# Performance work log

Hardware: AMD Instinct MI355X
Metric: run time of the kernel (lower is better)

The kernel has to match this reference:

```python
import jax, jax.numpy as jnp
from jax import lax
import numpy as np

BINS = 25
K = 5  # entropy patch size
EPS = 1e-5


def conv2d(x, w, b, stride, pad):
    y = lax.conv_general_dilated(x, w, (stride, stride), [(pad, pad), (pad, pad)],
                                 dimension_numbers=("NCHW", "OIHW", "NCHW"))
    return y + b[None, :, None, None]


def group_norm_per_channel(x, w, b):
    # GroupNorm with num_groups == num_channels: per-channel norm over H,W (biased var)
    mu = x.mean(axis=(2, 3), keepdims=True)
    v = x.var(axis=(2, 3), keepdims=True)
    return (x - mu) / jnp.sqrt(v + EPS) * w[None, :, None, None] + b[None, :, None, None]


def channel_entropy(x):
    # x: (b,c,h,w). Unfold into 5x5 patches, per-patch histc(bins=25) over patch
    # values using that patch's min/max range (torch.histc default), then entropy.
    b, c, h, w = x.shape
    ho, wo = h - K + 1, w - K + 1
    # (b,c,K*K,L) -- fixed 25-position loop, vectorized over all data dims
    patches = jnp.stack([x[:, :, i:i + ho, j:j + wo]
                         for i in range(K) for j in range(K)], axis=2)
    patches = patches.reshape(b, c, K * K, ho * wo)
    mn = patches.min(axis=2, keepdims=True)
    mx = patches.max(axis=2, keepdims=True)
    rng = jnp.where(mx > mn, mx - mn, jnp.ones_like(mx))
    bins = jnp.clip(jnp.floor((patches - mn) / rng * BINS), 0, BINS - 1).astype(jnp.int32)
    # histogram via comparison one-hot: (b,c,L,BINS)
    counts = (bins[..., None] == jnp.arange(BINS, dtype=jnp.int32)).sum(axis=2)
    pk = counts.astype(x.dtype) / (K * K)
    ent = (-pk * jnp.log(jnp.clip(pk, 1e-5, 1.0 - 1e-5))).sum(axis=-1).mean(axis=-1)  # (b,c)
    return ent[:, :, None, None]


def instance_norm_ent(x, w, b):
    ent = channel_entropy(lax.stop_gradient(x))
    mu = x.mean(axis=(2, 3), keepdims=True)
    n = x.shape[2] * x.shape[3]
    v = x.var(axis=(2, 3), keepdims=True) * (n / (n - 1))  # unbiased var (torch default)
    return (x - mu) / jnp.sqrt(v + EPS) * w[None, :, None, None] * ent + b[None, :, None, None]


def setup_inputs() -> dict:
    key = jax.random.key(0)
    ks = jax.random.split(key, 24)
    s = 0.05
    d = {
        "x": jax.random.normal(ks[0], (64, 3, 224, 224), jnp.float32),
        "conv0_w": jax.random.normal(ks[1], (8, 3, 7, 7), jnp.float32) * s,
        "conv0_b": jax.random.normal(ks[2], (8,), jnp.float32) * s,
        "conv1_w": jax.random.normal(ks[3], (16, 8, 5, 5), jnp.float32) * s,
        "conv1_b": jax.random.normal(ks[4], (16,), jnp.float32) * s,
        "conv2_w": jax.random.normal(ks[5], (32, 16, 3, 3), jnp.float32) * s,
        "conv2_b": jax.random.normal(ks[6], (32,), jnp.float32) * s,
        "gn0_w": jnp.ones((8,), jnp.float32) + jax.random.normal(ks[7], (8,), jnp.float32) * s,
        "gn0_b": jax.random.normal(ks[8], (8,), jnp.float32) * s,
        "n1_w": jnp.ones((16,), jnp.float32) + jax.random.normal(ks[9], (16,), jnp.float32) * s,
        "n1_b": jax.random.normal(ks[10], (16,), jnp.float32) * s,
        "n2_w": jnp.ones((32,), jnp.float32) + jax.random.normal(ks[11], (32,), jnp.float32) * s,
        "n2_b": jax.random.normal(ks[12], (32,), jnp.float32) * s,
        "bn_g": jnp.ones((10368,), jnp.float32) + jax.random.normal(ks[13], (10368,), jnp.float32) * s,
        "bn_b": jax.random.normal(ks[14], (10368,), jnp.float32) * s,
        "fc1_w": jax.random.normal(ks[15], (32, 10368), jnp.float32) * 0.01,
        "fc1_b": jax.random.normal(ks[16], (32,), jnp.float32) * s,
        "shape_w": jax.random.normal(ks[17], (5, 32), jnp.float32) * s,
        "shape_b": jax.random.normal(ks[18], (5,), jnp.float32) * s,
        "vern_w": jax.random.normal(ks[19], (2, 32), jnp.float32) * s,
        "vern_b": jax.random.normal(ks[20], (2,), jnp.float32) * s,
    }
    return d


def reference(x, conv0_w, conv0_b, conv1_w, conv1_b, conv2_w, conv2_b,
              gn0_w, gn0_b, n1_w, n1_b, n2_w, n2_b,
              bn_g, bn_b, fc1_w, fc1_b, shape_w, shape_b, vern_w, vern_b):
    h = conv2d(x, conv0_w, conv0_b, 4, 2)          # (b,8,56,56)
    h = jax.nn.relu(group_norm_per_channel(h, gn0_w, gn0_b))
    h = conv2d(h, conv1_w, conv1_b, 3, 1)          # (b,16,18,18)
    h = jax.nn.relu(instance_norm_ent(h, n1_w, n1_b))
    h = conv2d(h, conv2_w, conv2_b, 1, 1)          # (b,32,18,18)
    h = jax.nn.relu(instance_norm_ent(h, n2_w, n2_b))
    h = h.reshape(h.shape[0], -1)                  # (b,10368)
    # BatchNorm1d (training mode: batch stats, biased var)
    mu = h.mean(axis=0)
    v = h.var(axis=0)
    h = (h - mu) / jnp.sqrt(v + EPS) * bn_g + bn_b
    h = jax.nn.relu(h @ fc1_w.T + fc1_b)           # (b,32)
    out_shape = jax.nn.softmax(h @ shape_w.T + shape_b, axis=-1)
    out_vern = jax.nn.softmax(h @ vern_w.T + vern_b, axis=-1)
    return (out_shape, out_vern)
```

## Files before the change

### kernel.cpp

```cpp
#include <hip/hip_runtime.h>
#include <math.h>

#define EPSD 1e-5


__device__ __forceinline__ double waveReduceSumD(double v) {
#pragma unroll
    for (int off = 32; off > 0; off >>= 1)
        v += __shfl_down(v, off, 64);
    return v;
}

template <int NW>
__device__ __forceinline__ double blockReduceSumD(double v, double* buf) {
    int lane = threadIdx.x & 63;
    int w = threadIdx.x >> 6;
    v = waveReduceSumD(v);
    __syncthreads();
    if (lane == 0) buf[w] = v;
    __syncthreads();
    double tot = 0.0;
#pragma unroll
    for (int i = 0; i < NW; i++) tot += buf[i];
    return tot;
}

__device__ __forceinline__ void build_ent_tab(float* tab) {
    int t = threadIdx.x;
    if (t < 26) {
        if (t == 0) tab[0] = 0.f;
        else {
            double pk = (double)t / 25.0;
            double cl = fmin(fmax(pk, 1e-5), 1.0 - 1e-5);
            tab[t] = (float)(-pk * log(cl));
        }
    }
}

__device__ __forceinline__ float patch_ent(const float* ch, int py, int px, const float* tab) {
    float pv[25];
#pragma unroll
    for (int i = 0; i < 5; i++)
#pragma unroll
        for (int j = 0; j < 5; j++)
            pv[i * 5 + j] = ch[(py + i) * 18 + px + j];
    float mn = pv[0], mx = pv[0];
#pragma unroll
    for (int k = 1; k < 25; k++) { mn = fminf(mn, pv[k]); mx = fmaxf(mx, pv[k]); }
    float rng = (mx > mn) ? (mx - mn) : 1.0f;
    unsigned long long a0 = 0ull, a1 = 0ull;
    int a2 = 0;
#pragma unroll
    for (int k = 0; k < 25; k++) {
        float tt = (pv[k] - mn) / rng * 25.0f;
        int bi = (int)floorf(tt);
        bi = bi < 0 ? 0 : (bi > 24 ? 24 : bi);
        unsigned sh0 = ((unsigned)(5 * bi)) & 63u;
        unsigned sh1 = ((unsigned)(5 * bi - 60)) & 63u;
        a0 += (bi < 12) ? (1ull << sh0) : 0ull;
        a1 += (bi >= 12 && bi < 24) ? (1ull << sh1) : 0ull;
        a2 += (bi == 24) ? 1 : 0;
    }
    float ent = 0.f;
#pragma unroll
    for (int k = 0; k < 12; k++) ent += tab[(a0 >> (5 * k)) & 31ull];
#pragma unroll
    for (int k = 0; k < 12; k++) ent += tab[(a1 >> (5 * k)) & 31ull];
    ent += tab[a2];
    return ent;
}

__global__ __launch_bounds__(128, 4) void k_conv0(const float* __restrict__ x,
                                                  const float* __restrict__ w,
                                                  const float* __restrict__ bias,
                                                  float* __restrict__ h0raw,
                                                  double* __restrict__ part0) {
    __shared__ __align__(16) float tile[2508];
    __shared__ double redbuf[2][16];
    int tl = blockIdx.x;
    int b = blockIdx.y;
    int t = threadIdx.x;
    for (int i = t; i < 2508; i += 128) tile[i] = 0.f;
    int y_base = tl * 8 - 2;
    const float* xb = x + (size_t)b * 150528;
    float acc[8];
#pragma unroll
    for (int c = 0; c < 8; c++) acc[c] = bias[c];
    int ry = t / 56, ox = t % 56;
    for (int ci = 0; ci < 3; ci++) {
        __syncthreads();
        for (int i = t; i < 616; i += 128) {
            int r = i / 56, f4 = i % 56;
            int yIn = y_base + r;
            if (yIn >= 0 && yIn < 224) {
                float4 v = *(const float4*)&xb[ci * 50176 + yIn * 224 + f4 * 4];
                float* tp = tile + r * 228;
                tp[114 + f4] = v.x;
                tp[171 + f4] = v.y;
                tp[f4 + 1]   = v.z;
                tp[58 + f4]  = v.w;
            }
        }
        __syncthreads();
        if (t < 112) {
            const float* wci = w + ci * 49;
#pragma unroll
            for (int ky = 0; ky < 7; ky++) {
                const float* rp = tile + (4 * ry + ky) * 228;
#pragma unroll
                for (int kx = 0; kx < 7; kx++) {
                    float v = rp[(kx & 3) * 57 + ox + (kx >> 2)];
#pragma unroll
                    for (int c = 0; c < 8; c++)
                        acc[c] += v * wci[c * 147 + ky * 7 + kx];
                }
            }
        }
    }
    if (t < 112) {
        int oy = tl * 2 + ry;
        int opix = oy * 56 + ox;
#pragma unroll
        for (int c = 0; c < 8; c++)
            h0raw[((size_t)b * 8 + c) * 3136 + opix] = acc[c];
    } else {
#pragma unroll
        for (int c = 0; c < 8; c++) acc[c] = 0.f;
    }
    int wv = t >> 6, lane = t & 63;
#pragma unroll
    for (int c = 0; c < 8; c++) {
        double rs = waveReduceSumD((double)acc[c]);
        double rq = waveReduceSumD((double)acc[c] * (double)acc[c]);
        if (lane == 0) { redbuf[wv][c * 2] = rs; redbuf[wv][c * 2 + 1] = rq; }
    }
    __syncthreads();
    if (t < 16) {
        double tot = redbuf[0][t] + redbuf[1][t];
        part0[(((size_t)b * 28 + tl) << 4) + t] = tot;
    }
}

__global__ __launch_bounds__(1024) void k_conv1_ent(const float* __restrict__ h0raw,
                                                    const double* __restrict__ part0,
                                                    const float* __restrict__ gw,
                                                    const float* __restrict__ gb,
                                                    const float* __restrict__ w,
                                                    const float* __restrict__ bias,
                                                    const float* __restrict__ nw,
                                                    const float* __restrict__ nb,
                                                    float* __restrict__ h1) {
    __shared__ __align__(16) float xin2[25088];
    __shared__ float vals[1296];
    __shared__ float tab[26];
    __shared__ float gnp[16];
    __shared__ double redbuf[16][2];
    __shared__ double entbuf[16];
    __shared__ float prm[4][3];
    int b = blockIdx.x >> 2;
    int grp = blockIdx.x & 3;
    int t = threadIdx.x;
    if (t < 8) {
        double s = 0.0, s2 = 0.0;
        const double* p = part0 + ((size_t)b * 28) * 16;
        for (int tile = 0; tile < 28; tile++) {
            s += p[tile * 16 + t * 2];
            s2 += p[tile * 16 + t * 2 + 1];
        }
        double mean = s / 3136.0;
        double var = s2 / 3136.0 - mean * mean;
        double rstd = 1.0 / sqrt(var + EPSD);
        double sc = (double)gw[t] * rstd;
        gnp[t] = (float)sc;
        gnp[8 + t] = (float)((double)gb[t] - mean * sc);
    }
    build_ent_tab(tab);
    __syncthreads();
    for (int i = t; i < 25088; i += 1024) {
        int ci = i / 3136, px = i - ci * 3136;
        float v = fmaxf(h0raw[(size_t)b * 25088 + i] * gnp[ci] + gnp[8 + ci], 0.f);
        xin2[(ci >> 1) * 6272 + px * 2 + (ci & 1)] = v;
    }
    __syncthreads();

    int wv = t >> 6, lane = t & 63;
    int c = wv >> 2;
    int q = wv & 3;
    int j_u = __builtin_amdgcn_readfirstlane(grp * 4 + c);
    const float* wg = w + (size_t)j_u * 200;
    float* vch = vals + c * 324;
    float bv = bias[j_u];
    double s = 0.0, s2 = 0.0;
    for (int p = q * 81 + lane; p < q * 81 + 81; p += 64) {
        int oy = p / 18, ox = p - oy * 18;
        int y0 = oy * 3 - 1, x0 = ox * 3 - 1;
        float acc = bv;
        if (oy >= 1 && ox >= 1) {
#pragma unroll
            for (int c2 = 0; c2 < 4; c2++) {
                const float* xp = xin2 + c2 * 6272 + (y0 * 56 + x0) * 2;
                const float* wp0 = wg + (2 * c2) * 25;
#pragma unroll
                for (int ky = 0; ky < 5; ky++)
#pragma unroll
                    for (int kx = 0; kx < 5; kx++) {
                        float2 v = *(const float2*)&xp[(ky * 56 + kx) * 2];
                        acc += v.x * wp0[ky * 5 + kx];
                        acc += v.y * wp0[25 + ky * 5 + kx];
                    }
            }
        } else {
            int ky0 = y0 < 0 ? 1 : 0;
            int kx0 = x0 < 0 ? 1 : 0;
            for (int c2 = 0; c2 < 4; c2++) {
                const float* xp = xin2 + c2 * 6272;
                const float* wp0 = wg + (2 * c2) * 25;
                for (int ky = ky0; ky < 5; ky++) {
                    for (int kx = kx0; kx < 5; kx++) {
                        float2 v = *(const float2*)&xp[((y0 + ky) * 56 + x0 + kx) * 2];
                        acc += v.x * wp0[ky * 5 + kx];
                        acc += v.y * wp0[25 + ky * 5 + kx];
                    }
                }
            }
        }
        vch[p] = acc;
        s += (double)acc; s2 += (double)acc * (double)acc;
    }
    s = waveReduceSumD(s);
    s2 = waveReduceSumD(s2);
    if (lane == 0) { redbuf[wv][0] = s; redbuf[wv][1] = s2; }
    __syncthreads();
    double ent = 0.0;
    if (lane < 49) {
        int pi = q * 49 + lane;
        ent = (double)patch_ent(vch, pi / 14, pi % 14, tab);
    }
    ent = waveReduceSumD(ent);
    if (lane == 0) entbuf[wv] = ent;
    __syncthreads();
    if (t < 4) {
        double ss = 0.0, qq = 0.0, ee = 0.0;
        for (int k = 0; k < 4; k++) {
            ss += redbuf[t * 4 + k][0];
            qq += redbuf[t * 4 + k][1];
            ee += entbuf[t * 4 + k];
        }
        double entmean = ee / 196.0;
        double mean = ss / 324.0;
        double varb = qq / 324.0 - mean * mean;
        double varu = varb * (324.0 / 323.0);
        double rstd = 1.0 / sqrt(varu + EPSD);
        prm[t][0] = (float)mean;
        prm[t][1] = (float)((double)nw[grp * 4 + t] * entmean * rstd);
        prm[t][2] = nb[grp * 4 + t];
    }
    __syncthreads();
    float* outp = h1 + ((size_t)b * 16 + grp * 4) * 324;
    for (int i = t; i < 1296; i += 1024) {
        int cc = i / 324;
        outp[i] = fmaxf((vals[i] - prm[cc][0]) * prm[cc][1] + prm[cc][2], 0.f);
    }
}

__global__ __launch_bounds__(256) void k_conv2_ent(const float* __restrict__ in,
                                                   const float* __restrict__ w,
                                                   const float* __restrict__ bias,
                                                   const float* __restrict__ nw,
                                                   const float* __restrict__ nb,
                                                   float* __restrict__ out) {
    __shared__ __align__(16) float xin2[5184];
    __shared__ float vals[324];
    __shared__ float tab[26];
    __shared__ double rbuf[4];
    int b = blockIdx.x >> 5;
    int c = blockIdx.x & 31;
    int t = threadIdx.x;
    const float* xb = in + (size_t)b * 5184;
    for (int i = t; i < 5184; i += 256) {
        int ci = i / 324, px = i - ci * 324;
        xin2[(ci >> 1) * 648 + px * 2 + (ci & 1)] = xb[i];
    }
    build_ent_tab(tab);
    __syncthreads();
    const float* wc = w + c * 144;
    float bv = bias[c];
    double s = 0.0, s2 = 0.0;
    {
        int oy = 1 + (t >> 4), ox = 1 + (t & 15);
        int base = ((oy - 1) * 18 + (ox - 1)) * 2;
        float acc = bv;
#pragma unroll
        for (int c2 = 0; c2 < 8; c2++) {
            const float* xp = xin2 + c2 * 648 + base;
            const float* wp = wc + c2 * 18;
#pragma unroll
            for (int ky = 0; ky < 3; ky++)
#pragma unroll
                for (int kx = 0; kx < 3; kx++) {
                    float2 v = *(const float2*)&xp[(ky * 18 + kx) * 2];
                    acc += v.x * wp[ky * 3 + kx];
                    acc += v.y * wp[9 + ky * 3 + kx];
                }
        }
        vals[oy * 18 + ox] = acc;
        s += (double)acc; s2 += (double)acc * (double)acc;
    }
    if (t < 68) {
        int oy, ox;
        if (t < 18)      { oy = 0;      ox = t; }
        else if (t < 36) { oy = 17;     ox = t - 18; }
        else if (t < 52) { oy = t - 35; ox = 0; }
        else             { oy = t - 51; ox = 17; }
        int y0 = oy - 1, x0 = ox - 1;
        int ky0 = y0 < 0 ? 1 : 0;
        int ky1 = (18 - y0) < 3 ? 2 : 3;
        int kx0 = x0 < 0 ? 1 : 0;
        int kx1 = (18 - x0) < 3 ? 2 : 3;
        float acc = bv;
        for (int c2 = 0; c2 < 8; c2++) {
            const float* xp = xin2 + c2 * 648;
            const float* wp = wc + c2 * 18;
            for (int ky = ky0; ky < ky1; ky++) {
                for (int kx = kx0; kx < kx1; kx++) {
                    float2 v = *(const float2*)&xp[((y0 + ky) * 18 + x0 + kx) * 2];
                    acc += v.x * wp[ky * 3 + kx];
                    acc += v.y * wp[9 + ky * 3 + kx];
                }
            }
        }
        vals[oy * 18 + ox] = acc;
        s += (double)acc; s2 += (double)acc * (double)acc;
    }
    __syncthreads();
    double ent = 0.0;
    if (t < 196) ent = (double)patch_ent(vals, t / 14, t % 14, tab);
    double entmean = blockReduceSumD<4>(ent, rbuf) / 196.0;
    double ssum  = blockReduceSumD<4>(s, rbuf);
    double s2sum = blockReduceSumD<4>(s2, rbuf);
    double mean = ssum / 324.0;
    double varb = s2sum / 324.0 - mean * mean;
    double varu = varb * (324.0 / 323.0);
    double rstd = 1.0 / sqrt(varu + EPSD);
    float sc = (float)((double)nw[c] * entmean * rstd);
    float mu = (float)mean;
    float be = nb[c];
    float* outp = out + ((size_t)b * 32 + c) * 324;
    for (int idx = t; idx < 324; idx += 256)
        outp[idx] = fmaxf((vals[idx] - mu) * sc + be, 0.f);
}

__global__ __launch_bounds__(256) void k_bnstats(const float* __restrict__ h2,
                                                 const float* __restrict__ g,
                                                 const float* __restrict__ bb,
                                                 float* __restrict__ scale,
                                                 float* __restrict__ shift) {
    __shared__ double sb[4][64], qb[4][64];
    int lane = threadIdx.x & 63;
    int q = threadIdx.x >> 6;
    int f = blockIdx.x * 64 + lane;
    double s = 0.0, s2 = 0.0;
    for (int b = q * 16; b < q * 16 + 16; b++) {
        double v = (double)h2[(size_t)b * 10368 + f];
        s += v; s2 += v * v;
    }
    sb[q][lane] = s; qb[q][lane] = s2;
    __syncthreads();
    if (threadIdx.x < 64) {
        double S = sb[0][lane] + sb[1][lane] + sb[2][lane] + sb[3][lane];
        double Q = qb[0][lane] + qb[1][lane] + qb[2][lane] + qb[3][lane];
        double mean = S / 64.0;
        double var = Q / 64.0 - mean * mean;
        double rstd = 1.0 / sqrt(var + EPSD);
        double sc = (double)g[f] * rstd;
        scale[f] = (float)sc;
        shift[f] = (float)((double)bb[f] - mean * sc);
    }
}

__global__ __launch_bounds__(256) void k_fc1(const float* __restrict__ h2,
                                             const float* __restrict__ scale,
                                             const float* __restrict__ shift,
                                             const float* __restrict__ w1,
                                             const float* __restrict__ b1,
                                             float* __restrict__ fcout) {
    __shared__ double rbuf[4];
    int b = blockIdx.x >> 5;
    int j = blockIdx.x & 31;
    const float* hb = h2 + (size_t)b * 10368;
    const float* wj = w1 + (size_t)j * 10368;
    double acc = 0.0;
    for (int f = threadIdx.x * 4; f < 10368; f += 1024) {
        float4 h4 = *(const float4*)&hb[f];
        float4 s4 = *(const float4*)&scale[f];
        float4 t4 = *(const float4*)&shift[f];
        float4 w4 = *(const float4*)&wj[f];
        acc += (double)((h4.x * s4.x + t4.x) * w4.x);
        acc += (double)((h4.y * s4.y + t4.y) * w4.y);
        acc += (double)((h4.z * s4.z + t4.z) * w4.z);
        acc += (double)((h4.w * s4.w + t4.w) * w4.w);
    }
    acc = blockReduceSumD<4>(acc, rbuf);
    if (threadIdx.x == 0)
        fcout[b * 32 + j] = (float)fmax(acc + (double)b1[j], 0.0);
}

__global__ __launch_bounds__(64) void k_heads(const float* __restrict__ fc,
                                              const float* __restrict__ sw,
                                              const float* __restrict__ sb,
                                              const float* __restrict__ vw,
                                              const float* __restrict__ vb,
                                              float* __restrict__ out) {
    int b = threadIdx.x;
    double h[32];
#pragma unroll
    for (int i = 0; i < 32; i++) h[i] = (double)fc[b * 32 + i];
    double lg[5];
    double mx = -1e300;
#pragma unroll
    for (int k = 0; k < 5; k++) {
        double a = (double)sb[k];
#pragma unroll
        for (int i = 0; i < 32; i++) a += h[i] * (double)sw[k * 32 + i];
        lg[k] = a;
        mx = fmax(mx, a);
    }
    double se = 0.0;
#pragma unroll
    for (int k = 0; k < 5; k++) { lg[k] = exp(lg[k] - mx); se += lg[k]; }
#pragma unroll
    for (int k = 0; k < 5; k++) out[b * 5 + k] = (float)(lg[k] / se);
    double l0 = (double)vb[0], l1 = (double)vb[1];
#pragma unroll
    for (int i = 0; i < 32; i++) { l0 += h[i] * (double)vw[i]; l1 += h[i] * (double)vw[32 + i]; }
    double m = fmax(l0, l1);
    double e0 = exp(l0 - m), e1 = exp(l1 - m);
    double inv = 1.0 / (e0 + e1);
    out[320 + b * 2 + 0] = (float)(e0 * inv);
    out[320 + b * 2 + 1] = (float)(e1 * inv);
}

extern "C" void kernel_launch(void* const* d_in, const int* in_sizes, int n_in,
                              void* d_out, int out_size, void* d_ws, size_t ws_size,
                              hipStream_t stream) {
    const float* x       = (const float*)d_in[0];
    const float* conv0_w = (const float*)d_in[1];
    const float* conv0_b = (const float*)d_in[2];
    const float* conv1_w = (const float*)d_in[3];
    const float* conv1_b = (const float*)d_in[4];
    const float* conv2_w = (const float*)d_in[5];
    const float* conv2_b = (const float*)d_in[6];
    const float* gn0_w   = (const float*)d_in[7];
    const float* gn0_b   = (const float*)d_in[8];
    const float* n1_w    = (const float*)d_in[9];
    const float* n1_b    = (const float*)d_in[10];
    const float* n2_w    = (const float*)d_in[11];
    const float* n2_b    = (const float*)d_in[12];
    const float* bn_g    = (const float*)d_in[13];
    const float* bn_b    = (const float*)d_in[14];
    const float* fc1_w   = (const float*)d_in[15];
    const float* fc1_b   = (const float*)d_in[16];
    const float* shape_w = (const float*)d_in[17];
    const float* shape_b = (const float*)d_in[18];
    const float* vern_w  = (const float*)d_in[19];
    const float* vern_b  = (const float*)d_in[20];
    float* out = (float*)d_out;

    double* part0 = (double*)d_ws;
    float* fbase   = (float*)(part0 + 28672);
    float* h0raw   = fbase;
    float* h1      = h0raw + 1605632;
    float* h2      = h1 + 331776;
    float* bnscale = h2 + 663552;
    float* bnshift = bnscale + 10368;
    float* fc      = bnshift + 10368;

    k_conv0<<<dim3(28, 64), dim3(128), 0, stream>>>(x, conv0_w, conv0_b, h0raw, part0);
    k_conv1_ent<<<dim3(256), dim3(1024), 0, stream>>>(h0raw, part0, gn0_w, gn0_b,
                                                      conv1_w, conv1_b, n1_w, n1_b, h1);
    k_conv2_ent<<<dim3(2048), dim3(256), 0, stream>>>(h1, conv2_w, conv2_b, n2_w, n2_b, h2);
    k_bnstats<<<dim3(162), dim3(256), 0, stream>>>(h2, bn_g, bn_b, bnscale, bnshift);
    k_fc1<<<dim3(2048), dim3(256), 0, stream>>>(h2, bnscale, bnshift, fc1_w, fc1_b, fc);
    k_heads<<<dim3(1), dim3(64), 0, stream>>>(fc, shape_w, shape_b, vern_w, vern_b, out);
}
```

Before: 224.6 us.

## Fuse fc1 and softmax heads into one per-sample kernel with LDS-staged activations

Replaces the 2048-block fc1 kernel and the single-block heads kernel with one kernel that uses a 1024-thread block per sample. Each block normalizes the sample's activations into shared memory once. Each wave then computes two fc1 outputs and one thread evaluates both softmax heads. This removes one launch, the fc round trip through global memory, and the repeated per-output reads of h, scale and shift. In exchange only 64 blocks run, which lowers parallelism for streaming the fc1 weights. Separately, it also disables unrolling of the ky loop in conv0, likely to reduce register pressure.

```diff
diff --git a/kernel.cpp b/kernel.cpp
--- a/kernel.cpp
+++ b/kernel.cpp
@@ -104,7 +104,7 @@
         __syncthreads();
         if (t < 112) {
             const float* wci = w + ci * 49;
-#pragma unroll
+#pragma unroll 1
             for (int ky = 0; ky < 7; ky++) {
                 const float* rp = tile + (4 * ry + ky) * 228;
 #pragma unroll
@@ -378,66 +378,80 @@
     }
 }
 
-__global__ __launch_bounds__(256) void k_fc1(const float* __restrict__ h2,
-                                             const float* __restrict__ scale,
-                                             const float* __restrict__ shift,
-                                             const float* __restrict__ w1,
-                                             const float* __restrict__ b1,
-                                             float* __restrict__ fcout) {
-    __shared__ double rbuf[4];
-    int b = blockIdx.x >> 5;
-    int j = blockIdx.x & 31;
+__global__ __launch_bounds__(1024) void k_fc_heads(const float* __restrict__ h2,
+                                                   const float* __restrict__ scale,
+                                                   const float* __restrict__ shift,
+                                                   const float* __restrict__ w1,
+                                                   const float* __restrict__ b1,
+                                                   const float* __restrict__ sw,
+                                                   const float* __restrict__ sb,
+                                                   const float* __restrict__ vw,
+                                                   const float* __restrict__ vb,
+                                                   float* __restrict__ out) {
+    __shared__ __align__(16) float hv[10368];
+    __shared__ double dbuf[32];
+    int b = blockIdx.x;
+    int t = threadIdx.x;
     const float* hb = h2 + (size_t)b * 10368;
-    const float* wj = w1 + (size_t)j * 10368;
-    double acc = 0.0;
-    for (int f = threadIdx.x * 4; f < 10368; f += 1024) {
-        float4 h4 = *(const float4*)&hb[f];
-        float4 s4 = *(const float4*)&scale[f];
-        float4 t4 = *(const float4*)&shift[f];
-        float4 w4 = *(const float4*)&wj[f];
-        acc += (double)((h4.x * s4.x + t4.x) * w4.x);
-        acc += (double)((h4.y * s4.y + t4.y) * w4.y);
-        acc += (double)((h4.z * s4.z + t4.z) * w4.z);
-        acc += (double)((h4.w * s4.w + t4.w) * w4.w);
-    }
-    acc = blockReduceSumD<4>(acc, rbuf);
-    if (threadIdx.x == 0)
-        fcout[b * 32 + j] = (float)fmax(acc + (double)b1[j], 0.0);
-}
-
-__global__ __launch_bounds__(64) void k_heads(const float* __restrict__ fc,
-                                              const float* __restrict__ sw,
-                                              const float* __restrict__ sb,
-                                              const float* __restrict__ vw,
-                                              const float* __restrict__ vb,
-                                              float* __restrict__ out) {
-    int b = threadIdx.x;
-    double h[32];
-#pragma unroll
-    for (int i = 0; i < 32; i++) h[i] = (double)fc[b * 32 + i];
-    double lg[5];
-    double mx = -1e300;
-#pragma unroll
-    for (int k = 0; k < 5; k++) {
-        double a = (double)sb[k];
-#pragma unroll
-        for (int i = 0; i < 32; i++) a += h[i] * (double)sw[k * 32 + i];
-        lg[k] = a;
-        mx = fmax(mx, a);
-    }
-    double se = 0.0;
-#pragma unroll
-    for (int k = 0; k < 5; k++) { lg[k] = exp(lg[k] - mx); se += lg[k]; }
-#pragma unroll
-    for (int k = 0; k < 5; k++) out[b * 5 + k] = (float)(lg[k] / se);
-    double l0 = (double)vb[0], l1 = (double)vb[1];
-#pragma unroll
-    for (int i = 0; i < 32; i++) { l0 += h[i] * (double)vw[i]; l1 += h[i] * (double)vw[32 + i]; }
-    double m = fmax(l0, l1);
-    double e0 = exp(l0 - m), e1 = exp(l1 - m);
-    double inv = 1.0 / (e0 + e1);
-    out[320 + b * 2 + 0] = (float)(e0 * inv);
-    out[320 + b * 2 + 1] = (float)(e1 * inv);
+    for (int i = t * 4; i < 10368; i += 4096) {
+        float4 h4 = *(const float4*)&hb[i];
+        float4 s4 = *(const float4*)&scale[i];
+        float4 t4 = *(const float4*)&shift[i];
+        float4 r;
+        r.x = h4.x * s4.x + t4.x;
+        r.y = h4.y * s4.y + t4.y;
+        r.z = h4.z * s4.z + t4.z;
+        r.w = h4.w * s4.w + t4.w;
+        *(float4*)&hv[i] = r;
+    }
+    __syncthreads();
+    int wv = t >> 6, lane = t & 63;
+#pragma unroll
+    for (int k = 0; k < 2; k++) {
+        int j = wv * 2 + k;
+        const float* wj = w1 + (size_t)j * 10368;
+        double acc = 0.0;
+        for (int i = lane * 4; i < 10368; i += 256) {
+            float4 x4 = *(const float4*)&hv[i];
+            float4 w4 = *(const float4*)&wj[i];
+            acc += (double)(x4.x * w4.x);
+            acc += (double)(x4.y * w4.y);
+            acc += (double)(x4.z * w4.z);
+            acc += (double)(x4.w * w4.w);
+        }
+        acc = waveReduceSumD(acc);
+        if (lane == 0) dbuf[j] = acc;
+    }
+    __syncthreads();
+    if (t == 0) {
+        double h[32];
+#pragma unroll
+        for (int j = 0; j < 32; j++)
+            h[j] = (double)(float)fmax(dbuf[j] + (double)b1[j], 0.0);
+        double lg[5];
+        double mx = -1e300;
+#pragma unroll
+        for (int k = 0; k < 5; k++) {
+            double a = (double)sb[k];
+#pragma unroll
+            for (int i = 0; i < 32; i++) a += h[i] * (double)sw[k * 32 + i];
+            lg[k] = a;
+            mx = fmax(mx, a);
+        }
+        double se = 0.0;
+#pragma unroll
+        for (int k = 0; k < 5; k++) { lg[k] = exp(lg[k] - mx); se += lg[k]; }
+#pragma unroll
+        for (int k = 0; k < 5; k++) out[b * 5 + k] = (float)(lg[k] / se);
+        double l0 = (double)vb[0], l1 = (double)vb[1];
+#pragma unroll
+        for (int i = 0; i < 32; i++) { l0 += h[i] * (double)vw[i]; l1 += h[i] * (double)vw[32 + i]; }
+        double m = fmax(l0, l1);
+        double e0 = exp(l0 - m), e1 = exp(l1 - m);
+        double inv = 1.0 / (e0 + e1);
+        out[320 + b * 2 + 0] = (float)(e0 * inv);
+        out[320 + b * 2 + 1] = (float)(e1 * inv);
+    }
 }
 
 extern "C" void kernel_launch(void* const* d_in, const int* in_sizes, int n_in,
@@ -473,13 +487,12 @@
     float* h2      = h1 + 331776;
     float* bnscale = h2 + 663552;
     float* bnshift = bnscale + 10368;
-    float* fc      = bnshift + 10368;
 
     k_conv0<<<dim3(28, 64), dim3(128), 0, stream>>>(x, conv0_w, conv0_b, h0raw, part0);
     k_conv1_ent<<<dim3(256), dim3(1024), 0, stream>>>(h0raw, part0, gn0_w, gn0_b,
                                                       conv1_w, conv1_b, n1_w, n1_b, h1);
     k_conv2_ent<<<dim3(2048), dim3(256), 0, stream>>>(h1, conv2_w, conv2_b, n2_w, n2_b, h2);
     k_bnstats<<<dim3(162), dim3(256), 0, stream>>>(h2, bn_g, bn_b, bnscale, bnshift);
-    k_fc1<<<dim3(2048), dim3(256), 0, stream>>>(h2, bnscale, bnshift, fc1_w, fc1_b, fc);
-    k_heads<<<dim3(1), dim3(64), 0, stream>>>(fc, shape_w, shape_b, vern_w, vern_b, out);
-}
+    k_fc_heads<<<dim3(64), dim3(1024), 0, stream>>>(h2, bnscale, bnshift, fc1_w, fc1_b,
+                                                    shape_w, shape_b, vern_w, vern_b, out);
+}
```

Result: slower. 240.0 us (+6.9%).
